# Optimization experiments

Measured on AMD Instinct MI355X. Metric: run time of the kernel, lower is better.

The kernel has to match this reference:

```python
import jax, jax.numpy as jnp
import numpy as np

N = 50000        # nodes
E = 800000       # edges (avg degree 16)
D_IN = 128
HID = 128
K = 3


def cheb_edge_weights(row, col, n):
    # PyG ChebConv sym normalization with assumed lambda_max = 2.0:
    # L_hat = (2/lambda_max) * (I - D^-1/2 A D^-1/2) - I = -D^-1/2 A D^-1/2 (zero diagonal)
    mask = (row != col).astype(jnp.float32)  # remove_self_loops
    deg = jax.ops.segment_sum(mask, row, num_segments=n)
    dinv = jnp.where(deg > 0.0, jax.lax.rsqrt(jnp.maximum(deg, 1.0)), 0.0)
    return -dinv[row] * dinv[col] * mask  # [E]


def cheb_conv(x, row, col, w_edge, W, b, n):
    # Chebyshev recursion: Tx0=x, Tx1=L_hat x, Tx_k = 2 L_hat Tx_{k-1} - Tx_{k-2}
    def prop(h):  # sparse L_hat @ h via gather + segment_sum
        return jax.ops.segment_sum(w_edge[:, None] * h[col], row, num_segments=n)

    Tx0 = x
    out = Tx0 @ W[0]
    Tx1 = prop(Tx0)
    out = out + Tx1 @ W[1]
    for k in range(2, W.shape[0]):
        Tx2 = 2.0 * prop(Tx1) - Tx0
        out = out + Tx2 @ W[k]
        Tx0, Tx1 = Tx1, Tx2
    return out + b


def setup_inputs() -> dict:
    key = jax.random.key(0)
    ks = jax.random.split(key, 8)
    x = jax.random.normal(ks[0], (N, D_IN), dtype=jnp.float32)
    ei = jax.random.randint(ks[1], (2, E), 0, N, dtype=jnp.int32)
    s = 0.05
    W1 = jax.random.normal(ks[2], (K, D_IN, HID), dtype=jnp.float32) * s
    b1 = jnp.zeros((HID,), dtype=jnp.float32)
    W2 = jax.random.normal(ks[3], (K, HID, HID), dtype=jnp.float32) * s
    b2 = jnp.zeros((HID,), dtype=jnp.float32)
    W3 = jax.random.normal(ks[4], (K, HID, HID), dtype=jnp.float32) * s
    b3 = jnp.zeros((HID,), dtype=jnp.float32)
    return {"x": x, "ei": ei, "W1": W1, "b1": b1, "W2": W2, "b2": b2, "W3": W3, "b3": b3}


def reference(x, ei, W1, b1, W2, b2, W3, b3):
    row, col = ei[0], ei[1]
    w_edge = cheb_edge_weights(row, col, N)
    # layer chain: ChebConv -> ReLU -> dropout (eval mode: identity)
    h = jax.nn.relu(cheb_conv(x, row, col, w_edge, W1, b1, N))
    h = jax.nn.relu(cheb_conv(h, row, col, w_edge, W2, b2, N))
    h = jax.nn.relu(cheb_conv(h, row, col, w_edge, W3, b3, N))
    return h
```

## Files before the change

### kernel.cpp

```cpp
#include <hip/hip_runtime.h>
#include <hip/hip_bf16.h>

#define DFEAT 128

typedef short bf16x8 __attribute__((ext_vector_type(8)));
typedef float f32x4  __attribute__((ext_vector_type(4)));
typedef unsigned short u16x8 __attribute__((ext_vector_type(8)));

__device__ __forceinline__ unsigned bf16r(float f) {
    unsigned u = __float_as_uint(f);
    u += 0x7fffu + ((u >> 16) & 1u);
    return u >> 16;
}
__device__ __forceinline__ unsigned pack_bf16(float lo, float hi) {
    return bf16r(lo) | (bf16r(hi) << 16);
}

__global__ void deg_kernel(const int* __restrict__ ei, int* __restrict__ deg8, int E, int N) {
    int e = blockIdx.x * blockDim.x + threadIdx.x;
    if (e < E) {
        int r = ei[e];
        int c = ei[E + e];
        if (r != c) atomicAdd(&deg8[(blockIdx.x & 7) * N + r], 1);
    }
}

__global__ __launch_bounds__(1024) void scan1_kernel(const int* __restrict__ deg8,
                                                     int* __restrict__ poff,
                                                     int* __restrict__ row_ptr,
                                                     int* __restrict__ bsum,
                                                     float* __restrict__ dinv, int n) {
    __shared__ int wsums[16];
    int t = threadIdx.x;
    int idx = blockIdx.x * 1024 + t;
    int tot = 0;
    if (idx < n) {
        int run = 0;
        #pragma unroll
        for (int p = 0; p < 8; ++p) {
            int d = deg8[p * n + idx];
            poff[p * n + idx] = run;
            run += d;
        }
        tot = run;
        dinv[idx] = (tot > 0) ? rsqrtf((float)tot) : 0.f;
    }
    int vi = tot;
    #pragma unroll
    for (int off = 1; off < 64; off <<= 1) {
        int x = __shfl_up(vi, off);
        if ((t & 63) >= off) vi += x;
    }
    if ((t & 63) == 63) wsums[t >> 6] = vi;
    __syncthreads();
    if (t < 16) {
        int s = wsums[t];
        int si = s;
        #pragma unroll
        for (int off = 1; off < 16; off <<= 1) {
            int x = __shfl_up(si, off);
            if (t >= off) si += x;
        }
        wsums[t] = si - s;
        if (t == 15) bsum[blockIdx.x] = si;
    }
    __syncthreads();
    if (idx < n) row_ptr[idx + 1] = wsums[t >> 6] + vi;
}

__global__ void scan2_kernel(int* __restrict__ bsum, int nb) {
    int t = threadIdx.x;
    int carry = 0;
    for (int base = 0; base < nb; base += 64) {
        int v = (base + t < nb) ? bsum[base + t] : 0;
        int vi = v;
        #pragma unroll
        for (int off = 1; off < 64; off <<= 1) {
            int x = __shfl_up(vi, off);
            if (t >= off) vi += x;
        }
        if (base + t < nb) bsum[base + t] = carry + vi - v;
        carry += __shfl(vi, 63);
    }
}

__global__ __launch_bounds__(1024) void scan3_kernel(int* __restrict__ row_ptr,
                                                     const int* __restrict__ bsum, int n) {
    int idx = blockIdx.x * 1024 + threadIdx.x;
    if (idx == 0) row_ptr[0] = 0;
    if (idx < n) row_ptr[idx + 1] += bsum[blockIdx.x];
}

__global__ void fill_kernel(const int* __restrict__ ei, const int* __restrict__ row_ptr,
                            const int* __restrict__ poff, int* __restrict__ fillc8,
                            const float* __restrict__ dinv,
                            unsigned* __restrict__ e_cw, int E, int N) {
    int e = blockIdx.x * blockDim.x + threadIdx.x;
    if (e < E) {
        int r = ei[e];
        int c = ei[E + e];
        if (r != c) {
            int p = blockIdx.x & 7;
            int k = atomicAdd(&fillc8[p * N + r], 1);
            int pos = row_ptr[r] + poff[p * N + r] + k;
            float w = -dinv[r] * dinv[c];
            _Float16 hf = (_Float16)w;
            unsigned short wb;
            __builtin_memcpy(&wb, &hf, 2);
            e_cw[pos] = (unsigned)c | ((unsigned)wb << 16);
        }
    }
}

__global__ void xconv_kernel(const float2* __restrict__ x, unsigned* __restrict__ xb, int n2) {
    int id = blockIdx.x * blockDim.x + threadIdx.x;
    if (id < n2) {
        float2 v = x[id];
        xb[id] = pack_bf16(v.x, v.y);
    }
}

__global__ void wprep_kernel(const float* __restrict__ W1, const float* __restrict__ W2,
                             const float* __restrict__ W3, unsigned short* __restrict__ Wt) {
    int id = blockIdx.x * blockDim.x + threadIdx.x;
    const int PER = 3 * DFEAT * DFEAT;
    if (id < 3 * PER) {
        int layer = id / PER;
        int rem = id - layer * PER;
        const float* W = (layer == 0) ? W1 : ((layer == 1) ? W2 : W3);
        int seg = rem >> 14;
        int k   = (rem >> 7) & 127;
        int nn  = rem & 127;
        Wt[layer * PER + (seg << 14) + (nn << 7) + k] = (unsigned short)bf16r(W[rem]);
    }
}

__global__ __launch_bounds__(256) void prop_bf16_kernel(
    const unsigned* __restrict__ hin, const unsigned* __restrict__ sub,
    unsigned* __restrict__ hout,
    const int* __restrict__ row_ptr, const unsigned* __restrict__ e_cw,
    float alpha, int n)
{
    int wv = __builtin_amdgcn_readfirstlane(threadIdx.x >> 6);
    int node = blockIdx.x * 4 + wv;
    int t = threadIdx.x & 63;
    if (node >= n) return;
    int s = row_ptr[node];
    int e = row_ptr[node + 1];
    float a0 = 0.f, a1 = 0.f;
    int j = s;
    for (; j + 16 <= e; j += 16) {
        unsigned cw[16];
        #pragma unroll
        for (int q = 0; q < 16; ++q) cw[q] = e_cw[j + q];
        unsigned v[16];
        #pragma unroll
        for (int q = 0; q < 16; ++q)
            v[q] = hin[(size_t)(cw[q] & 0xffffu) * 64 + t];
        #pragma unroll
        for (int q = 0; q < 16; ++q) {
            unsigned short wb = (unsigned short)(cw[q] >> 16);
            _Float16 hf; __builtin_memcpy(&hf, &wb, 2);
            float w = (float)hf;
            a0 += w * __uint_as_float(v[q] << 16);
            a1 += w * __uint_as_float(v[q] & 0xffff0000u);
        }
    }
    for (; j + 4 <= e; j += 4) {
        unsigned cw[4];
        #pragma unroll
        for (int q = 0; q < 4; ++q) cw[q] = e_cw[j + q];
        unsigned v[4];
        #pragma unroll
        for (int q = 0; q < 4; ++q)
            v[q] = hin[(size_t)(cw[q] & 0xffffu) * 64 + t];
        #pragma unroll
        for (int q = 0; q < 4; ++q) {
            unsigned short wb = (unsigned short)(cw[q] >> 16);
            _Float16 hf; __builtin_memcpy(&hf, &wb, 2);
            float w = (float)hf;
            a0 += w * __uint_as_float(v[q] << 16);
            a1 += w * __uint_as_float(v[q] & 0xffff0000u);
        }
    }
    for (; j < e; ++j) {
        unsigned cwv = e_cw[j];
        unsigned short wb = (unsigned short)(cwv >> 16);
        _Float16 hf; __builtin_memcpy(&hf, &wb, 2);
        float w = (float)hf;
        unsigned v = hin[(size_t)(cwv & 0xffffu) * 64 + t];
        a0 += w * __uint_as_float(v << 16);
        a1 += w * __uint_as_float(v & 0xffff0000u);
    }
    a0 *= alpha; a1 *= alpha;
    if (sub) {
        unsigned v = sub[(size_t)node * 64 + t];
        a0 -= __uint_as_float(v << 16);
        a1 -= __uint_as_float(v & 0xffff0000u);
    }
    hout[(size_t)node * 64 + t] = pack_bf16(a0, a1);
}

#define WPAD 136
__global__ __launch_bounds__(256) void gemm3_mfma_kernel(
    const unsigned short* __restrict__ X0, const unsigned short* __restrict__ X1,
    const unsigned short* __restrict__ X2,
    const unsigned short* __restrict__ Wt, const float* __restrict__ bias,
    void* __restrict__ out, int n, int out_bf16)
{
    __shared__ unsigned short Ws[DFEAT * WPAD];
    const int t    = threadIdx.x;
    const int wave = t >> 6;
    const int lane = t & 63;
    const int quad = lane >> 4;
    const int l16  = lane & 15;

    const int row_base = blockIdx.x * 128 + wave * 32;
    int r0 = row_base + l16;       if (r0 >= n) r0 = n - 1;
    int r1 = row_base + 16 + l16;  if (r1 >= n) r1 = n - 1;

    const unsigned short* Xps[3] = {X0, X1, X2};

    f32x4 acc[2][8];
    #pragma unroll
    for (int tt = 0; tt < 2; ++tt)
        #pragma unroll
        for (int c = 0; c < 8; ++c) acc[tt][c] = (f32x4){0.f, 0.f, 0.f, 0.f};

    const int srow = t >> 1;
    const int shalf = (t & 1) * 64;

    #pragma unroll
    for (int seg = 0; seg < 3; ++seg) {
        __syncthreads();
        const unsigned short* Wp = Wt + (seg << 14);
        #pragma unroll
        for (int i = 0; i < 8; ++i) {
            *(u16x8*)&Ws[srow * WPAD + shalf + i * 8] =
                *(const u16x8*)&Wp[srow * DFEAT + shalf + i * 8];
        }
        __syncthreads();
        const unsigned short* A0 = Xps[seg] + (size_t)r0 * DFEAT;
        const unsigned short* A1 = Xps[seg] + (size_t)r1 * DFEAT;
        #pragma unroll
        for (int kk = 0; kk < 4; ++kk) {
            const int ko = kk * 32 + quad * 8;
            bf16x8 a0 = *(const bf16x8*)(A0 + ko);
            bf16x8 a1 = *(const bf16x8*)(A1 + ko);
            #pragma unroll
            for (int c = 0; c < 8; ++c) {
                bf16x8 b = *(const bf16x8*)&Ws[(c * 16 + l16) * WPAD + ko];
                acc[0][c] = __builtin_amdgcn_mfma_f32_16x16x32_bf16(a0, b, acc[0][c], 0, 0, 0);
                acc[1][c] = __builtin_amdgcn_mfma_f32_16x16x32_bf16(a1, b, acc[1][c], 0, 0, 0);
            }
        }
    }

    #pragma unroll
    for (int tt = 0; tt < 2; ++tt) {
        int orow0 = blockIdx.x * 128 + wave * 32 + tt * 16 + quad * 4;
        #pragma unroll
        for (int c = 0; c < 8; ++c) {
            int col = c * 16 + l16;
            float bv = bias[col];
            #pragma unroll
            for (int r = 0; r < 4; ++r) {
                int orow = orow0 + r;
                if (orow < n) {
                    float v = fmaxf(acc[tt][c][r] + bv, 0.f);
                    if (out_bf16)
                        ((unsigned short*)out)[(size_t)orow * DFEAT + col] = (unsigned short)bf16r(v);
                    else
                        ((float*)out)[(size_t)orow * DFEAT + col] = v;
                }
            }
        }
    }
}

extern "C" void kernel_launch(void* const* d_in, const int* in_sizes, int n_in,
                              void* d_out, int out_size, void* d_ws, size_t ws_size,
                              hipStream_t stream) {
    const float* x  = (const float*)d_in[0];
    const int*   ei = (const int*)d_in[1];
    const float* W1 = (const float*)d_in[2];
    const float* b1 = (const float*)d_in[3];
    const float* W2 = (const float*)d_in[4];
    const float* b2 = (const float*)d_in[5];
    const float* W3 = (const float*)d_in[6];
    const float* b3 = (const float*)d_in[7];

    const int N = in_sizes[0] / DFEAT;
    const int E = in_sizes[1] / 2;
    const int NPK = N * (DFEAT / 2);
    const int NB = (N + 1023) / 1024;

    unsigned* xb  = (unsigned*)d_ws;
    unsigned* t1b = xb  + NPK;
    unsigned* t2b = t1b + NPK;
    unsigned* ab  = t2b + NPK;
    unsigned short* wt = (unsigned short*)(ab + NPK);
    int*   deg8    = (int*)(wt + 3 * 3 * DFEAT * DFEAT);
    int*   poff    = deg8 + 8 * N;
    int*   fillc8  = poff + 8 * N;
    int*   row_ptr = fillc8 + 8 * N;
    float* dinv    = (float*)(row_ptr + (N + 1));
    unsigned* e_cw = (unsigned*)(dinv + N);
    int*   bsum    = (int*)(e_cw + E);

    hipMemsetAsync(deg8,   0, sizeof(int) * 8 * N, stream);
    hipMemsetAsync(fillc8, 0, sizeof(int) * 8 * N, stream);

    deg_kernel<<<(E + 255) / 256, 256, 0, stream>>>(ei, deg8, E, N);
    scan1_kernel<<<NB, 1024, 0, stream>>>(deg8, poff, row_ptr, bsum, dinv, N);
    scan2_kernel<<<1, 64, 0, stream>>>(bsum, NB);
    scan3_kernel<<<NB, 1024, 0, stream>>>(row_ptr, bsum, N);
    fill_kernel<<<(E + 255) / 256, 256, 0, stream>>>(ei, row_ptr, poff, fillc8, dinv, e_cw, E, N);

    xconv_kernel<<<(NPK + 255) / 256, 256, 0, stream>>>((const float2*)x, xb, NPK);
    const int WELEM = 3 * DFEAT * DFEAT;
    wprep_kernel<<<(3 * WELEM + 255) / 256, 256, 0, stream>>>(W1, W2, W3, wt);

    const float* bl[3] = {b1, b2, b3};
    const unsigned* hin = xb;
    const int prop_grid = (N + 3) / 4;
    const int gemm_grid = (N + 127) / 128;
    for (int l = 0; l < 3; ++l) {
        prop_bf16_kernel<<<prop_grid, 256, 0, stream>>>(hin, nullptr, t1b, row_ptr, e_cw, 1.f, N);
        prop_bf16_kernel<<<prop_grid, 256, 0, stream>>>(t1b, hin, t2b, row_ptr, e_cw, 2.f, N);
        void* hout = (l == 2) ? d_out : (void*)ab;
        gemm3_mfma_kernel<<<gemm_grid, 256, 0, stream>>>(
            (const unsigned short*)hin, (const unsigned short*)t1b, (const unsigned short*)t2b,
            wt + l * WELEM, bl[l], hout, N, (l == 2) ? 0 : 1);
        hin = ab;
    }
}
```

Before: 409.5 us.

## Process four nodes per wave with 16-byte gathers in SpMM propagation

Rewrites the propagation kernel so each wave handles four nodes, with 16 lanes per node each gathering a uint4 (8 bf16 features) instead of one dword per lane for a single node. Neighbors are processed in unrolled batches of six, iterating up to the maximum degree among the four nodes and masking lanes whose node has fewer edges. This aims to widen memory transactions and improve latency hiding on the irregular gather. The cost is divergence-driven wasted iterations when degrees differ within a wave, plus more registers for the eight accumulators.

```diff
diff --git a/kernel.cpp b/kernel.cpp
--- a/kernel.cpp
+++ b/kernel.cpp
@@ -15,6 +15,8 @@
 __device__ __forceinline__ unsigned pack_bf16(float lo, float hi) {
     return bf16r(lo) | (bf16r(hi) << 16);
 }
+__device__ __forceinline__ float blo(unsigned v) { return __uint_as_float(v << 16); }
+__device__ __forceinline__ float bhi(unsigned v) { return __uint_as_float(v & 0xffff0000u); }
 
 __global__ void deg_kernel(const int* __restrict__ ei, int* __restrict__ deg8, int E, int N) {
     int e = blockIdx.x * blockDim.x + threadIdx.x;
@@ -136,69 +138,66 @@
 }
 
 __global__ __launch_bounds__(256) void prop_bf16_kernel(
-    const unsigned* __restrict__ hin, const unsigned* __restrict__ sub,
-    unsigned* __restrict__ hout,
+    const uint4* __restrict__ hin4, const uint4* __restrict__ sub4,
+    uint4* __restrict__ hout4,
     const int* __restrict__ row_ptr, const unsigned* __restrict__ e_cw,
     float alpha, int n)
 {
-    int wv = __builtin_amdgcn_readfirstlane(threadIdx.x >> 6);
-    int node = blockIdx.x * 4 + wv;
-    int t = threadIdx.x & 63;
-    if (node >= n) return;
-    int s = row_ptr[node];
-    int e = row_ptr[node + 1];
-    float a0 = 0.f, a1 = 0.f;
-    int j = s;
-    for (; j + 16 <= e; j += 16) {
-        unsigned cw[16];
-        #pragma unroll
-        for (int q = 0; q < 16; ++q) cw[q] = e_cw[j + q];
-        unsigned v[16];
-        #pragma unroll
-        for (int q = 0; q < 16; ++q)
-            v[q] = hin[(size_t)(cw[q] & 0xffffu) * 64 + t];
-        #pragma unroll
-        for (int q = 0; q < 16; ++q) {
-            unsigned short wb = (unsigned short)(cw[q] >> 16);
+    const int t = threadIdx.x;
+    const int lane = t & 63;
+    const int q = lane >> 4;
+    const int s = lane & 15;
+    int node = blockIdx.x * 16 + (t >> 6) * 4 + q;
+    int nodec = node < n ? node : n - 1;
+    int rs = row_ptr[nodec];
+    int deg = row_ptr[nodec + 1] - rs;
+    if (node >= n) deg = 0;
+    int m = deg;
+    m = max(m, __shfl_xor(m, 16));
+    m = max(m, __shfl_xor(m, 32));
+
+    float acc[8];
+    #pragma unroll
+    for (int i = 0; i < 8; ++i) acc[i] = 0.f;
+
+    for (int i0 = 0; i0 < m; i0 += 6) {
+        uint4 vv[6]; float wv[6];
+        #pragma unroll
+        for (int u = 0; u < 6; ++u) {
+            int i = i0 + u;
+            unsigned cw = (i < deg) ? e_cw[rs + i] : 0u;
+            unsigned short wb = (unsigned short)(cw >> 16);
             _Float16 hf; __builtin_memcpy(&hf, &wb, 2);
-            float w = (float)hf;
-            a0 += w * __uint_as_float(v[q] << 16);
-            a1 += w * __uint_as_float(v[q] & 0xffff0000u);
-        }
-    }
-    for (; j + 4 <= e; j += 4) {
-        unsigned cw[4];
-        #pragma unroll
-        for (int q = 0; q < 4; ++q) cw[q] = e_cw[j + q];
-        unsigned v[4];
-        #pragma unroll
-        for (int q = 0; q < 4; ++q)
-            v[q] = hin[(size_t)(cw[q] & 0xffffu) * 64 + t];
-        #pragma unroll
-        for (int q = 0; q < 4; ++q) {
-            unsigned short wb = (unsigned short)(cw[q] >> 16);
-            _Float16 hf; __builtin_memcpy(&hf, &wb, 2);
-            float w = (float)hf;
-            a0 += w * __uint_as_float(v[q] << 16);
-            a1 += w * __uint_as_float(v[q] & 0xffff0000u);
-        }
-    }
-    for (; j < e; ++j) {
-        unsigned cwv = e_cw[j];
-        unsigned short wb = (unsigned short)(cwv >> 16);
-        _Float16 hf; __builtin_memcpy(&hf, &wb, 2);
-        float w = (float)hf;
-        unsigned v = hin[(size_t)(cwv & 0xffffu) * 64 + t];
-        a0 += w * __uint_as_float(v << 16);
-        a1 += w * __uint_as_float(v & 0xffff0000u);
-    }
-    a0 *= alpha; a1 *= alpha;
-    if (sub) {
-        unsigned v = sub[(size_t)node * 64 + t];
-        a0 -= __uint_as_float(v << 16);
-        a1 -= __uint_as_float(v & 0xffff0000u);
-    }
-    hout[(size_t)node * 64 + t] = pack_bf16(a0, a1);
+            wv[u] = (float)hf;
+            vv[u] = hin4[(size_t)(cw & 0xffffu) * 16 + s];
+        }
+        #pragma unroll
+        for (int u = 0; u < 6; ++u) {
+            float w = wv[u];
+            acc[0] += w * blo(vv[u].x);  acc[1] += w * bhi(vv[u].x);
+            acc[2] += w * blo(vv[u].y);  acc[3] += w * bhi(vv[u].y);
+            acc[4] += w * blo(vv[u].z);  acc[5] += w * bhi(vv[u].z);
+            acc[6] += w * blo(vv[u].w);  acc[7] += w * bhi(vv[u].w);
+        }
+    }
+    #pragma unroll
+    for (int i = 0; i < 8; ++i) acc[i] *= alpha;
+    size_t rowoff = (size_t)nodec * 16 + s;
+    if (sub4) {
+        uint4 sv = sub4[rowoff];
+        acc[0] -= blo(sv.x);  acc[1] -= bhi(sv.x);
+        acc[2] -= blo(sv.y);  acc[3] -= bhi(sv.y);
+        acc[4] -= blo(sv.z);  acc[5] -= bhi(sv.z);
+        acc[6] -= blo(sv.w);  acc[7] -= bhi(sv.w);
+    }
+    if (node < n) {
+        uint4 o;
+        o.x = pack_bf16(acc[0], acc[1]);
+        o.y = pack_bf16(acc[2], acc[3]);
+        o.z = pack_bf16(acc[4], acc[5]);
+        o.w = pack_bf16(acc[6], acc[7]);
+        hout4[rowoff] = o;
+    }
 }
 
 #define WPAD 136
@@ -323,11 +322,13 @@
 
     const float* bl[3] = {b1, b2, b3};
     const unsigned* hin = xb;
-    const int prop_grid = (N + 3) / 4;
+    const int prop_grid = (N + 15) / 16;
     const int gemm_grid = (N + 127) / 128;
     for (int l = 0; l < 3; ++l) {
-        prop_bf16_kernel<<<prop_grid, 256, 0, stream>>>(hin, nullptr, t1b, row_ptr, e_cw, 1.f, N);
-        prop_bf16_kernel<<<prop_grid, 256, 0, stream>>>(t1b, hin, t2b, row_ptr, e_cw, 2.f, N);
+        prop_bf16_kernel<<<prop_grid, 256, 0, stream>>>(
+            (const uint4*)hin, nullptr, (uint4*)t1b, row_ptr, e_cw, 1.f, N);
+        prop_bf16_kernel<<<prop_grid, 256, 0, stream>>>(
+            (const uint4*)t1b, (const uint4*)hin, (uint4*)t2b, row_ptr, e_cw, 2.f, N);
         void* hout = (l == 2) ? d_out : (void*)ab;
         gemm3_mfma_kernel<<<gemm_grid, 256, 0, stream>>>(
             (const unsigned short*)hin, (const unsigned short*)t1b, (const unsigned short*)t2b,
```

After: 438.4 us. +7.1%, slower.
